# Performance work log

Hardware: AMD Instinct MI355X
Metric: run time of the kernel (lower is better)

Reference implementation:

```python
import jax, jax.numpy as jnp
import numpy as np

K = 1024
D = 512
BETA = 0.25
ALPHA = 10.0
EPS_NORM = 1e-12  # torch F.normalize eps


def _l2_normalize(x):
    n = jnp.linalg.norm(x, axis=1, keepdims=True)
    return x / jnp.maximum(n, EPS_NORM)


def setup_inputs() -> dict:
    key = jax.random.key(0)
    k1, k2 = jax.random.split(key)
    latents = jax.random.normal(k1, (16384, D), dtype=jnp.float32)
    # nn.Embedding weight init: uniform(-1/K, 1/K)
    emb_weight = jax.random.uniform(k2, (K, D), dtype=jnp.float32,
                                    minval=-1.0 / K, maxval=1.0 / K)
    return {"latents": latents, "emb_weight": emb_weight}


def reference(latents, emb_weight):
    # latents: [B, D], emb_weight: [K, D]
    ln = _l2_normalize(latents)                               # [B, D]
    # torch uses embedding.weight.data -> detached for the attention path
    cb = _l2_normalize(jax.lax.stop_gradient(emb_weight))     # [K, D]
    attention = ln @ cb.T                                     # [B, K]
    soft_assign = jax.nn.softmax(ALPHA * attention, axis=1)   # [B, K]
    quantized = soft_assign @ emb_weight                      # [B, D]

    commitment_loss = jnp.mean((jax.lax.stop_gradient(quantized) - ln) ** 2)
    embedding_loss = jnp.mean((quantized - jax.lax.stop_gradient(ln)) ** 2)
    vq_loss = commitment_loss * BETA + embedding_loss

    avg_probs = jnp.mean(soft_assign, axis=0)                 # [K]
    entropy_vq = -jnp.sum(avg_probs * jnp.log(avg_probs + 1e-10))

    argm = jnp.argmax(attention, axis=1, keepdims=True)       # [B, 1] int
    one_hot = jax.nn.one_hot(argm[:, 0], K, dtype=latents.dtype)  # [B, K]
    hard_quantized = one_hot @ emb_weight                     # [B, D]
    # attention[one_hot.bool()].mean() == mean of row-max (argmax entries)
    cluster_metric = jnp.mean(jnp.max(attention, axis=1))

    return (quantized, vq_loss, entropy_vq, argm, hard_quantized,
            soft_assign, cluster_metric)
```

## Files before the change

### kernel.cpp

```cpp
#include <hip/hip_runtime.h>
#include <math.h>

#define D     512
#define KCB   1024
#define NT    256
#define NT2   512
#define ALPHA 10.0f
#define TAU   0.008f

typedef __attribute__((ext_vector_type(8))) short short8v;
typedef __attribute__((ext_vector_type(4))) float f32x4;
typedef unsigned short us;

__device__ __forceinline__ float wave_reduce_sum(float v) {
    #pragma unroll
    for (int off = 32; off >= 1; off >>= 1) v += __shfl_xor(v, off, 64);
    return v;
}

__device__ __forceinline__ short bf16r(float x) {
    union { float f; unsigned u; } c; c.f = x;
    unsigned r = (c.u + 0x7FFFu + ((c.u >> 16) & 1u)) >> 16;
    return (short)r;
}

__global__ void k_init(float* __restrict__ avg, float* __restrict__ sse, float* __restrict__ clu) {
    int t = threadIdx.x + blockIdx.x * blockDim.x;
    if (t < KCB) avg[t] = 0.0f;
    if (t == 0) { *sse = 0.0f; *clu = 0.0f; }
}

__global__ __launch_bounds__(NT) void k_prep(const float* __restrict__ emb,
                                             us* __restrict__ cb, float* __restrict__ cbinv) {
    const int k = blockIdx.x, t = threadIdx.x;
    const int wv = t >> 6, lane = t & 63;
    float2 v = ((const float2*)(emb + (size_t)k * D))[t];
    float ss = wave_reduce_sum(v.x * v.x + v.y * v.y);
    __shared__ float part[4];
    __shared__ float s_i;
    if (lane == 0) part[wv] = ss;
    __syncthreads();
    if (t == 0) s_i = 1.0f / fmaxf(sqrtf(part[0] + part[1] + part[2] + part[3]), 1e-12f);
    __syncthreads();
    float inv = s_i;
    unsigned lo = (unsigned short)bf16r(v.x * inv);
    unsigned hi = (unsigned short)bf16r(v.y * inv);
    const int d = 2 * t;
    size_t idx = (((size_t)(k >> 4) * 16 + (d >> 5)) * 64 + ((d >> 3) & 3) * 16 + (k & 15)) * 8 + (d & 7);
    ((unsigned*)cb)[idx >> 1] = lo | (hi << 16);
    if (t == 0) cbinv[k] = inv;
}

__global__ __launch_bounds__(NT) void k_tr(const float* __restrict__ emb, us* __restrict__ embT) {
    __shared__ us tile[64][65];
    const int t = threadIdx.x;
    const int k0 = (blockIdx.x & 15) * 64;
    const int d0 = (blockIdx.x >> 4) * 64;
    {
        const int r = t >> 2, cq = t & 3;
        const float4* ep = (const float4*)(emb + (size_t)(k0 + r) * D + d0 + cq * 16);
        float4 v0 = ep[0], v1 = ep[1], v2 = ep[2], v3 = ep[3];
        us* tp = &tile[r][cq * 16];
        tp[0] = (us)bf16r(v0.x); tp[1] = (us)bf16r(v0.y); tp[2] = (us)bf16r(v0.z); tp[3] = (us)bf16r(v0.w);
        tp[4] = (us)bf16r(v1.x); tp[5] = (us)bf16r(v1.y); tp[6] = (us)bf16r(v1.z); tp[7] = (us)bf16r(v1.w);
        tp[8] = (us)bf16r(v2.x); tp[9] = (us)bf16r(v2.y); tp[10] = (us)bf16r(v2.z); tp[11] = (us)bf16r(v2.w);
        tp[12] = (us)bf16r(v3.x); tp[13] = (us)bf16r(v3.y); tp[14] = (us)bf16r(v3.z); tp[15] = (us)bf16r(v3.w);
    }
    __syncthreads();
    {
        const int rd = t >> 2, kq = t & 3;
        const int dcol = d0 + rd;
        short8v w0, w1;
        #pragma unroll
        for (int j = 0; j < 8; ++j) w0[j] = (short)tile[kq * 16 + j][rd];
        #pragma unroll
        for (int j = 0; j < 8; ++j) w1[j] = (short)tile[kq * 16 + 8 + j][rd];
        const int kb0 = k0 + kq * 16, kb1 = kb0 + 8;
        size_t i0 = (((size_t)(dcol >> 4) * 32 + (kb0 >> 5)) * 64 + ((kb0 >> 3) & 3) * 16 + (dcol & 15)) * 8;
        size_t i1 = (((size_t)(dcol >> 4) * 32 + (kb1 >> 5)) * 64 + ((kb1 >> 3) & 3) * 16 + (dcol & 15)) * 8;
        *(short8v*)(embT + i0) = w0;
        *(short8v*)(embT + i1) = w1;
    }
}

__global__ __launch_bounds__(NT2, 2) void k_attn(
    const float* __restrict__ lat, const float* __restrict__ emb,
    const us* __restrict__ cb, const float* __restrict__ cbinv,
    float* __restrict__ inv_ws, float* __restrict__ avg_ws, float* __restrict__ clu_ws,
    float* __restrict__ soft_out, float* __restrict__ argm_out, float* __restrict__ hq_out)
{
    __shared__ __align__(16) us alds[32][520];
    __shared__ float s_inv[32];
    __shared__ float s_maxp[8][32];
    __shared__ float s_amax[32];
    __shared__ float s_sump[8][32];
    __shared__ float s_den[32];
    __shared__ float s_bestv[32];
    __shared__ int   s_besti[32];
    __shared__ int   s_cnt;
    __shared__ int   s_ck[512];
    __shared__ float s_cv[512];

    const int t = threadIdx.x, wv = t >> 6, lane = t & 63;
    const int q15 = lane & 15, g = lane >> 4;
    const int b0 = blockIdx.x * 32;

    #pragma unroll
    for (int i = 0; i < 4; ++i) {
        int r = wv * 4 + i, grow = b0 + r;
        const float4* lp = (const float4*)(lat + (size_t)grow * D);
        float4 a = lp[2 * lane], b = lp[2 * lane + 1];
        float ss = a.x*a.x + a.y*a.y + a.z*a.z + a.w*a.w
                 + b.x*b.x + b.y*b.y + b.z*b.z + b.w*b.w;
        ss = wave_reduce_sum(ss);
        float inv = 1.0f / fmaxf(sqrtf(ss), 1e-12f);
        short8v w;
        w[0] = bf16r(a.x * inv); w[1] = bf16r(a.y * inv);
        w[2] = bf16r(a.z * inv); w[3] = bf16r(a.w * inv);
        w[4] = bf16r(b.x * inv); w[5] = bf16r(b.y * inv);
        w[6] = bf16r(b.z * inv); w[7] = bf16r(b.w * inv);
        *(short8v*)&alds[r][lane * 8] = w;
        if (lane == 0) { s_inv[r] = inv; inv_ws[grow] = inv; }
    }
    if (t == 0) s_cnt = 0;
    __syncthreads();

    f32x4 acc[2][8];
    #pragma unroll
    for (int m = 0; m < 2; ++m)
        #pragma unroll
        for (int ct = 0; ct < 8; ++ct) { f32x4 z = {0.f, 0.f, 0.f, 0.f}; acc[m][ct] = z; }

    const us* pBw = cb + (size_t)(wv * 8) * 16 * 512 + (size_t)lane * 8;
    for (int ks = 0; ks < 16; ++ks) {
        short8v af0 = *(const short8v*)&alds[q15][ks * 32 + g * 8];
        short8v af1 = *(const short8v*)&alds[16 + q15][ks * 32 + g * 8];
        short8v bfr[8];
        #pragma unroll
        for (int ct = 0; ct < 8; ++ct)
            bfr[ct] = *(const short8v*)(pBw + (size_t)(ct * 16 + ks) * 512);
        #pragma unroll
        for (int ct = 0; ct < 8; ++ct) {
            acc[0][ct] = __builtin_amdgcn_mfma_f32_16x16x32_bf16(af0, bfr[ct], acc[0][ct], 0, 0, 0);
            acc[1][ct] = __builtin_amdgcn_mfma_f32_16x16x32_bf16(af1, bfr[ct], acc[1][ct], 0, 0, 0);
        }
    }

    #pragma unroll
    for (int m = 0; m < 2; ++m)
        #pragma unroll
        for (int i = 0; i < 4; ++i) {
            float v = acc[m][0][i];
            #pragma unroll
            for (int ct = 1; ct < 8; ++ct) v = fmaxf(v, acc[m][ct][i]);
            #pragma unroll
            for (int off = 8; off >= 1; off >>= 1) v = fmaxf(v, __shfl_xor(v, off, 64));
            if (q15 == 0) s_maxp[wv][m * 16 + g * 4 + i] = v;
        }
    __syncthreads();
    if (t < 32) {
        float v = s_maxp[0][t];
        #pragma unroll
        for (int w = 1; w < 8; ++w) v = fmaxf(v, s_maxp[w][t]);
        s_amax[t] = v;
    }
    __syncthreads();

    #pragma unroll
    for (int m = 0; m < 2; ++m)
        #pragma unroll
        for (int i = 0; i < 4; ++i) {
            const int row = m * 16 + g * 4 + i;
            const float thr = s_amax[row] - TAU;
            #pragma unroll
            for (int ct = 0; ct < 8; ++ct) {
                if (acc[m][ct][i] >= thr) {
                    int idx = atomicAdd(&s_cnt, 1);
                    if (idx < 512) s_ck[idx] = (row << 16) | (wv * 128 + ct * 16 + q15);
                }
            }
        }
    __syncthreads();
    const int cnt = (s_cnt < 512) ? s_cnt : 512;

    for (int e = wv; e < cnt; e += 8) {
        const int pk = s_ck[e];
        const int row = pk >> 16, kk = pk & 0xFFFF;
        const float4* lp = (const float4*)(lat + (size_t)(b0 + row) * D);
        const float4* ep = (const float4*)(emb + (size_t)kk * D);
        float4 x0 = lp[2 * lane], x1 = lp[2 * lane + 1];
        float4 y0 = ep[2 * lane], y1 = ep[2 * lane + 1];
        float dp = x0.x*y0.x + x0.y*y0.y + x0.z*y0.z + x0.w*y0.w
                 + x1.x*y1.x + x1.y*y1.y + x1.z*y1.z + x1.w*y1.w;
        dp = wave_reduce_sum(dp);
        if (lane == 0) s_cv[e] = dp * s_inv[row] * cbinv[kk];
    }
    __syncthreads();
    if (t < 32) {
        float bv = -1e30f; int bi = 0x7FFFFFFF;
        for (int e = 0; e < cnt; ++e) {
            if ((s_ck[e] >> 16) == t) {
                float v = s_cv[e]; int kk = s_ck[e] & 0xFFFF;
                if (v > bv || (v == bv && kk < bi)) { bv = v; bi = kk; }
            }
        }
        s_bestv[t] = bv; s_besti[t] = bi;
        argm_out[b0 + t] = (float)bi;
    }
    __syncthreads();

    #pragma unroll
    for (int m = 0; m < 2; ++m)
        #pragma unroll
        for (int i = 0; i < 4; ++i) {
            const float bvv = s_bestv[m * 16 + g * 4 + i];
            float s = 0.f;
            #pragma unroll
            for (int ct = 0; ct < 8; ++ct) {
                float e = __expf(ALPHA * (acc[m][ct][i] - bvv));
                acc[m][ct][i] = e;
                s += e;
            }
            #pragma unroll
            for (int off = 8; off >= 1; off >>= 1) s += __shfl_xor(s, off, 64);
            if (q15 == 0) s_sump[wv][m * 16 + g * 4 + i] = s;
        }
    __syncthreads();
    if (t < 32) {
        float s = s_sump[0][t];
        #pragma unroll
        for (int w = 1; w < 8; ++w) s += s_sump[w][t];
        s_den[t] = 1.0f / s;
    }
    __syncthreads();

    float csum[8];
    #pragma unroll
    for (int ct = 0; ct < 8; ++ct) csum[ct] = 0.f;
    #pragma unroll
    for (int m = 0; m < 2; ++m)
        #pragma unroll
        for (int i = 0; i < 4; ++i) {
            const int row = m * 16 + g * 4 + i;
            const float dn = s_den[row];
            float* orow = soft_out + (size_t)(b0 + row) * KCB + wv * 128 + q15;
            #pragma unroll
            for (int ct = 0; ct < 8; ++ct) {
                float sv = acc[m][ct][i] * dn;
                orow[ct * 16] = sv;
                csum[ct] += sv;
            }
        }
    #pragma unroll
    for (int ct = 0; ct < 8; ++ct) {
        float v = csum[ct];
        v += __shfl_xor(v, 16, 64);
        v += __shfl_xor(v, 32, 64);
        csum[ct] = v;
    }
    if (lane < 16) {
        #pragma unroll
        for (int ct = 0; ct < 8; ++ct)
            atomicAdd(avg_ws + wv * 128 + ct * 16 + lane, csum[ct]);
    }
    if (t == 0) {
        float cs = 0.f;
        #pragma unroll
        for (int r = 0; r < 32; ++r) cs += s_bestv[r];
        atomicAdd(clu_ws, cs);
    }

    const float4* emb4 = (const float4*)emb;
    for (int idx = t; idx < 32 * 128; idx += NT2) {
        int r = idx >> 7, c = idx & 127;
        ((float4*)(hq_out + (size_t)(b0 + r) * D))[c] = emb4[(size_t)s_besti[r] * 128 + c];
    }
}

__global__ __launch_bounds__(NT2, 2) void k_quant(
    const float* __restrict__ lat, const us* __restrict__ embT,
    const float* __restrict__ soft_in, const float* __restrict__ inv_ws,
    float* __restrict__ q_out, float* __restrict__ sse_ws)
{
    __shared__ __align__(16) us salds[32][516];
    __shared__ float part[8];
    const int t = threadIdx.x, wv = t >> 6, lane = t & 63;
    const int q15 = lane & 15, g = lane >> 4;
    const int b0 = blockIdx.x * 32;

    f32x4 acc[2][4];
    #pragma unroll
    for (int m = 0; m < 2; ++m)
        #pragma unroll
        for (int ct = 0; ct < 4; ++ct) { f32x4 z = {0.f, 0.f, 0.f, 0.f}; acc[m][ct] = z; }

    const float4* s4 = (const float4*)soft_in;
    for (int p = 0; p < 2; ++p) {
        for (int idx = t; idx < 32 * 128; idx += NT2) {
            int r = idx >> 7, c4 = idx & 127;
            float4 v = s4[(size_t)(b0 + r) * (KCB / 4) + p * 128 + c4];
            uint2 u;
            u.x = (unsigned)(us)bf16r(v.x) | ((unsigned)(us)bf16r(v.y) << 16);
            u.y = (unsigned)(us)bf16r(v.z) | ((unsigned)(us)bf16r(v.w) << 16);
            *(uint2*)&salds[r][c4 * 4] = u;
        }
        __syncthreads();

        const us* pBw = embT + ((size_t)(wv * 128) + p * 16) * 512 + (size_t)lane * 8;
        for (int ks = 0; ks < 16; ++ks) {
            short8v af0 = *(const short8v*)&salds[q15][ks * 32 + g * 8];
            short8v af1 = *(const short8v*)&salds[16 + q15][ks * 32 + g * 8];
            short8v bfr[4];
            #pragma unroll
            for (int ct = 0; ct < 4; ++ct)
                bfr[ct] = *(const short8v*)(pBw + (size_t)(ct * 32 + ks) * 512);
            #pragma unroll
            for (int ct = 0; ct < 4; ++ct) {
                acc[0][ct] = __builtin_amdgcn_mfma_f32_16x16x32_bf16(af0, bfr[ct], acc[0][ct], 0, 0, 0);
                acc[1][ct] = __builtin_amdgcn_mfma_f32_16x16x32_bf16(af1, bfr[ct], acc[1][ct], 0, 0, 0);
            }
        }
        __syncthreads();
    }

    float sse = 0.f;
    #pragma unroll
    for (int m = 0; m < 2; ++m)
        #pragma unroll
        for (int i = 0; i < 4; ++i) {
            const int row = b0 + m * 16 + g * 4 + i;
            const float rv = inv_ws[row];
            const float* lrow = lat + (size_t)row * D + wv * 64 + q15;
            float* qrow = q_out + (size_t)row * D + wv * 64 + q15;
            #pragma unroll
            for (int ct = 0; ct < 4; ++ct) {
                float qv = acc[m][ct][i];
                qrow[ct * 16] = qv;
                float df = qv - lrow[ct * 16] * rv;
                sse += df * df;
            }
        }
    sse = wave_reduce_sum(sse);
    if (lane == 0) part[wv] = sse;
    __syncthreads();
    if (t == 0) {
        float s = 0.f;
        #pragma unroll
        for (int w = 0; w < 8; ++w) s += part[w];
        atomicAdd(sse_ws, s);
    }
}

__global__ __launch_bounds__(NT) void k_final(
    const float* __restrict__ avg_ws, const float* __restrict__ sse_ws, const float* __restrict__ clu_ws,
    float* __restrict__ out_vq, float* __restrict__ out_ent, float* __restrict__ out_cm,
    float invB, float invBD)
{
    const int t = threadIdx.x;
    float ent = 0.f;
    for (int idx = t; idx < KCB; idx += NT) {
        float pv = avg_ws[idx] * invB;
        ent -= pv * logf(pv + 1e-10f);
    }
    ent = wave_reduce_sum(ent);
    __shared__ float part[4];
    const int wv = t >> 6, lane = t & 63;
    if (lane == 0) part[wv] = ent;
    __syncthreads();
    if (t == 0) {
        *out_ent = part[0] + part[1] + part[2] + part[3];
        *out_vq  = 1.25f * (*sse_ws) * invBD;
        *out_cm  = (*clu_ws) * invB;
    }
}

extern "C" void kernel_launch(void* const* d_in, const int* in_sizes, int n_in,
                              void* d_out, int out_size, void* d_ws, size_t ws_size,
                              hipStream_t stream)
{
    const float* lat = (const float*)d_in[0];
    const float* emb = (const float*)d_in[1];
    const int B = in_sizes[0] / D;
    float* out = (float*)d_out;

    const size_t vq_off   = (size_t)B * D;
    const size_t ent_off  = vq_off + 1;
    const size_t argm_off = vq_off + 2;
    const size_t hq_off   = argm_off + (size_t)B;
    const size_t soft_off = hq_off + (size_t)B * D;
    const size_t cm_off   = soft_off + (size_t)B * KCB;

    us* cb_bf   = (us*)d_ws;
    us* embT_bf = cb_bf + (size_t)KCB * D;
    float* fbase  = (float*)(embT_bf + (size_t)D * KCB);
    float* inv_ws = fbase;
    float* cbinv  = inv_ws + B;
    float* avg_ws = cbinv + KCB;
    float* sse_ws = avg_ws + KCB;
    float* clu_ws = sse_ws + 1;

    k_init<<<4, NT, 0, stream>>>(avg_ws, sse_ws, clu_ws);
    k_prep<<<KCB, NT, 0, stream>>>(emb, cb_bf, cbinv);
    k_tr<<<(D / 64) * (KCB / 64), NT, 0, stream>>>(emb, embT_bf);
    k_attn<<<B / 32, NT2, 0, stream>>>(lat, emb, cb_bf, cbinv, inv_ws, avg_ws, clu_ws,
                                       out + soft_off, out + argm_off, out + hq_off);
    k_quant<<<B / 32, NT2, 0, stream>>>(lat, embT_bf, out + soft_off, inv_ws, out, sse_ws);
    k_final<<<1, NT, 0, stream>>>(avg_ws, sse_ws, clu_ws,
                                  out + vq_off, out + ent_off, out + cm_off,
                                  1.0f / (float)B, 1.0f / ((float)B * (float)D));
}
```

Before: 299.1 us.

## Fuse attention and quantize kernels, keeping soft-assign tile in LDS as bf16

Merges k_attn and k_quant into one kernel. The softmax probabilities are written as bf16 into a dynamic LDS pool and consumed directly by the second GEMM, so the 64MB soft_assign tensor no longer has to be re-read from global memory and the inv_ws round trip is gone. It also double-buffers the B-fragment global loads in both GEMM loops so loads overlap the MFMAs. In exchange the fused kernel carries more LDS (about 66KB of dynamic LDS) and more registers, which may lower occupancy, and the two GEMMs now run serially within each block.

```diff
diff --git a/kernel.cpp b/kernel.cpp
--- a/kernel.cpp
+++ b/kernel.cpp
@@ -7,6 +7,7 @@
 #define NT2   512
 #define ALPHA 10.0f
 #define TAU   0.008f
+#define PSTR  1040
 
 typedef __attribute__((ext_vector_type(8))) short short8v;
 typedef __attribute__((ext_vector_type(4))) float f32x4;
@@ -83,13 +84,14 @@
     }
 }
 
-__global__ __launch_bounds__(NT2, 2) void k_attn(
+__global__ __launch_bounds__(NT2, 2) void k_fused(
     const float* __restrict__ lat, const float* __restrict__ emb,
-    const us* __restrict__ cb, const float* __restrict__ cbinv,
-    float* __restrict__ inv_ws, float* __restrict__ avg_ws, float* __restrict__ clu_ws,
-    float* __restrict__ soft_out, float* __restrict__ argm_out, float* __restrict__ hq_out)
+    const us* __restrict__ cb, const us* __restrict__ embT, const float* __restrict__ cbinv,
+    float* __restrict__ avg_ws, float* __restrict__ clu_ws, float* __restrict__ sse_ws,
+    float* __restrict__ q_out, float* __restrict__ soft_out,
+    float* __restrict__ argm_out, float* __restrict__ hq_out)
 {
-    __shared__ __align__(16) us alds[32][520];
+    extern __shared__ __align__(16) us pool[];
     __shared__ float s_inv[32];
     __shared__ float s_maxp[8][32];
     __shared__ float s_amax[32];
@@ -100,16 +102,22 @@
     __shared__ int   s_cnt;
     __shared__ int   s_ck[512];
     __shared__ float s_cv[512];
+    __shared__ float part[8];
 
     const int t = threadIdx.x, wv = t >> 6, lane = t & 63;
     const int q15 = lane & 15, g = lane >> 4;
     const int b0 = blockIdx.x * 32;
 
+    float4 ra[4], rb[4];
     #pragma unroll
     for (int i = 0; i < 4; ++i) {
-        int r = wv * 4 + i, grow = b0 + r;
-        const float4* lp = (const float4*)(lat + (size_t)grow * D);
-        float4 a = lp[2 * lane], b = lp[2 * lane + 1];
+        const float4* lp = (const float4*)(lat + (size_t)(b0 + wv * 4 + i) * D);
+        ra[i] = lp[2 * lane]; rb[i] = lp[2 * lane + 1];
+    }
+    #pragma unroll
+    for (int i = 0; i < 4; ++i) {
+        int r = wv * 4 + i;
+        float4 a = ra[i], b = rb[i];
         float ss = a.x*a.x + a.y*a.y + a.z*a.z + a.w*a.w
                  + b.x*b.x + b.y*b.y + b.z*b.z + b.w*b.w;
         ss = wave_reduce_sum(ss);
@@ -119,8 +127,8 @@
         w[2] = bf16r(a.z * inv); w[3] = bf16r(a.w * inv);
         w[4] = bf16r(b.x * inv); w[5] = bf16r(b.y * inv);
         w[6] = bf16r(b.z * inv); w[7] = bf16r(b.w * inv);
-        *(short8v*)&alds[r][lane * 8] = w;
-        if (lane == 0) { s_inv[r] = inv; inv_ws[grow] = inv; }
+        *(short8v*)&pool[(size_t)r * PSTR + lane * 8] = w;
+        if (lane == 0) s_inv[r] = inv;
     }
     if (t == 0) s_cnt = 0;
     __syncthreads();
@@ -132,17 +140,29 @@
         for (int ct = 0; ct < 8; ++ct) { f32x4 z = {0.f, 0.f, 0.f, 0.f}; acc[m][ct] = z; }
 
     const us* pBw = cb + (size_t)(wv * 8) * 16 * 512 + (size_t)lane * 8;
-    for (int ks = 0; ks < 16; ++ks) {
-        short8v af0 = *(const short8v*)&alds[q15][ks * 32 + g * 8];
-        short8v af1 = *(const short8v*)&alds[16 + q15][ks * 32 + g * 8];
-        short8v bfr[8];
-        #pragma unroll
-        for (int ct = 0; ct < 8; ++ct)
-            bfr[ct] = *(const short8v*)(pBw + (size_t)(ct * 16 + ks) * 512);
+    #define LDB_A(ks, ct) (*(const short8v*)(pBw + (size_t)((ct) * 16 + (ks)) * 512))
+    #define LDA_A(row, ks) (*(const short8v*)&pool[(size_t)(row) * PSTR + (ks) * 32 + g * 8])
+
+    short8v bE[8], bO[8];
+    #pragma unroll
+    for (int ct = 0; ct < 8; ++ct) bE[ct] = LDB_A(0, ct);
+    for (int ks = 0; ks < 16; ks += 2) {
+        #pragma unroll
+        for (int ct = 0; ct < 8; ++ct) bO[ct] = LDB_A(ks + 1, ct);
+        short8v af0 = LDA_A(q15, ks), af1 = LDA_A(16 + q15, ks);
         #pragma unroll
         for (int ct = 0; ct < 8; ++ct) {
-            acc[0][ct] = __builtin_amdgcn_mfma_f32_16x16x32_bf16(af0, bfr[ct], acc[0][ct], 0, 0, 0);
-            acc[1][ct] = __builtin_amdgcn_mfma_f32_16x16x32_bf16(af1, bfr[ct], acc[1][ct], 0, 0, 0);
+            acc[0][ct] = __builtin_amdgcn_mfma_f32_16x16x32_bf16(af0, bE[ct], acc[0][ct], 0, 0, 0);
+            acc[1][ct] = __builtin_amdgcn_mfma_f32_16x16x32_bf16(af1, bE[ct], acc[1][ct], 0, 0, 0);
+        }
+        const int ksn = (ks + 2 < 16) ? ks + 2 : 0;
+        #pragma unroll
+        for (int ct = 0; ct < 8; ++ct) bE[ct] = LDB_A(ksn, ct);
+        af0 = LDA_A(q15, ks + 1); af1 = LDA_A(16 + q15, ks + 1);
+        #pragma unroll
+        for (int ct = 0; ct < 8; ++ct) {
+            acc[0][ct] = __builtin_amdgcn_mfma_f32_16x16x32_bf16(af0, bO[ct], acc[0][ct], 0, 0, 0);
+            acc[1][ct] = __builtin_amdgcn_mfma_f32_16x16x32_bf16(af1, bO[ct], acc[1][ct], 0, 0, 0);
         }
     }
 
@@ -244,10 +264,12 @@
             const int row = m * 16 + g * 4 + i;
             const float dn = s_den[row];
             float* orow = soft_out + (size_t)(b0 + row) * KCB + wv * 128 + q15;
+            us* prow = &pool[(size_t)row * PSTR + wv * 128 + q15];
             #pragma unroll
             for (int ct = 0; ct < 8; ++ct) {
                 float sv = acc[m][ct][i] * dn;
                 orow[ct * 16] = sv;
+                prow[ct * 16] = (us)bf16r(sv);
                 csum[ct] += sv;
             }
         }
@@ -269,58 +291,47 @@
         for (int r = 0; r < 32; ++r) cs += s_bestv[r];
         atomicAdd(clu_ws, cs);
     }
+    __syncthreads();
 
     const float4* emb4 = (const float4*)emb;
-    for (int idx = t; idx < 32 * 128; idx += NT2) {
+    #pragma unroll
+    for (int u = 0; u < 8; ++u) {
+        int idx = t + u * NT2;
         int r = idx >> 7, c = idx & 127;
         ((float4*)(hq_out + (size_t)(b0 + r) * D))[c] = emb4[(size_t)s_besti[r] * 128 + c];
     }
-}
-
-__global__ __launch_bounds__(NT2, 2) void k_quant(
-    const float* __restrict__ lat, const us* __restrict__ embT,
-    const float* __restrict__ soft_in, const float* __restrict__ inv_ws,
-    float* __restrict__ q_out, float* __restrict__ sse_ws)
-{
-    __shared__ __align__(16) us salds[32][516];
-    __shared__ float part[8];
-    const int t = threadIdx.x, wv = t >> 6, lane = t & 63;
-    const int q15 = lane & 15, g = lane >> 4;
-    const int b0 = blockIdx.x * 32;
-
-    f32x4 acc[2][4];
-    #pragma unroll
-    for (int m = 0; m < 2; ++m)
-        #pragma unroll
-        for (int ct = 0; ct < 4; ++ct) { f32x4 z = {0.f, 0.f, 0.f, 0.f}; acc[m][ct] = z; }
-
-    const float4* s4 = (const float4*)soft_in;
-    for (int p = 0; p < 2; ++p) {
-        for (int idx = t; idx < 32 * 128; idx += NT2) {
-            int r = idx >> 7, c4 = idx & 127;
-            float4 v = s4[(size_t)(b0 + r) * (KCB / 4) + p * 128 + c4];
-            uint2 u;
-            u.x = (unsigned)(us)bf16r(v.x) | ((unsigned)(us)bf16r(v.y) << 16);
-            u.y = (unsigned)(us)bf16r(v.z) | ((unsigned)(us)bf16r(v.w) << 16);
-            *(uint2*)&salds[r][c4 * 4] = u;
-        }
-        __syncthreads();
-
-        const us* pBw = embT + ((size_t)(wv * 128) + p * 16) * 512 + (size_t)lane * 8;
-        for (int ks = 0; ks < 16; ++ks) {
-            short8v af0 = *(const short8v*)&salds[q15][ks * 32 + g * 8];
-            short8v af1 = *(const short8v*)&salds[16 + q15][ks * 32 + g * 8];
-            short8v bfr[4];
-            #pragma unroll
-            for (int ct = 0; ct < 4; ++ct)
-                bfr[ct] = *(const short8v*)(pBw + (size_t)(ct * 32 + ks) * 512);
-            #pragma unroll
-            for (int ct = 0; ct < 4; ++ct) {
-                acc[0][ct] = __builtin_amdgcn_mfma_f32_16x16x32_bf16(af0, bfr[ct], acc[0][ct], 0, 0, 0);
-                acc[1][ct] = __builtin_amdgcn_mfma_f32_16x16x32_bf16(af1, bfr[ct], acc[1][ct], 0, 0, 0);
-            }
-        }
-        __syncthreads();
+
+    f32x4 qac[2][4];
+    #pragma unroll
+    for (int m = 0; m < 2; ++m)
+        #pragma unroll
+        for (int ct = 0; ct < 4; ++ct) { f32x4 z = {0.f, 0.f, 0.f, 0.f}; qac[m][ct] = z; }
+
+    const us* pBq = embT + (size_t)(wv * 128) * 512 + (size_t)lane * 8;
+    #define LDB_Q(ks, ct) (*(const short8v*)(pBq + (size_t)((ct) * 32 + (ks)) * 512))
+    #define LDA_Q(row, ks) (*(const short8v*)&pool[(size_t)(row) * PSTR + (ks) * 32 + g * 8])
+
+    short8v qE[4], qO[4];
+    #pragma unroll
+    for (int ct = 0; ct < 4; ++ct) qE[ct] = LDB_Q(0, ct);
+    for (int ks = 0; ks < 32; ks += 2) {
+        #pragma unroll
+        for (int ct = 0; ct < 4; ++ct) qO[ct] = LDB_Q(ks + 1, ct);
+        short8v af0 = LDA_Q(q15, ks), af1 = LDA_Q(16 + q15, ks);
+        #pragma unroll
+        for (int ct = 0; ct < 4; ++ct) {
+            qac[0][ct] = __builtin_amdgcn_mfma_f32_16x16x32_bf16(af0, qE[ct], qac[0][ct], 0, 0, 0);
+            qac[1][ct] = __builtin_amdgcn_mfma_f32_16x16x32_bf16(af1, qE[ct], qac[1][ct], 0, 0, 0);
+        }
+        const int ksn = (ks + 2 < 32) ? ks + 2 : 0;
+        #pragma unroll
+        for (int ct = 0; ct < 4; ++ct) qE[ct] = LDB_Q(ksn, ct);
+        af0 = LDA_Q(q15, ks + 1); af1 = LDA_Q(16 + q15, ks + 1);
+        #pragma unroll
+        for (int ct = 0; ct < 4; ++ct) {
+            qac[0][ct] = __builtin_amdgcn_mfma_f32_16x16x32_bf16(af0, qO[ct], qac[0][ct], 0, 0, 0);
+            qac[1][ct] = __builtin_amdgcn_mfma_f32_16x16x32_bf16(af1, qO[ct], qac[1][ct], 0, 0, 0);
+        }
     }
 
     float sse = 0.f;
@@ -328,13 +339,14 @@
     for (int m = 0; m < 2; ++m)
         #pragma unroll
         for (int i = 0; i < 4; ++i) {
-            const int row = b0 + m * 16 + g * 4 + i;
-            const float rv = inv_ws[row];
+            const int rloc = m * 16 + g * 4 + i;
+            const int row = b0 + rloc;
+            const float rv = s_inv[rloc];
             const float* lrow = lat + (size_t)row * D + wv * 64 + q15;
             float* qrow = q_out + (size_t)row * D + wv * 64 + q15;
             #pragma unroll
             for (int ct = 0; ct < 4; ++ct) {
-                float qv = acc[m][ct][i];
+                float qv = qac[m][ct][i];
                 qrow[ct * 16] = qv;
                 float df = qv - lrow[ct * 16] * rv;
                 sse += df * df;
@@ -349,6 +361,10 @@
         for (int w = 0; w < 8; ++w) s += part[w];
         atomicAdd(sse_ws, s);
     }
+    #undef LDB_A
+    #undef LDA_A
+    #undef LDB_Q
+    #undef LDA_Q
 }
 
 __global__ __launch_bounds__(NT) void k_final(
@@ -393,18 +409,19 @@
     us* cb_bf   = (us*)d_ws;
     us* embT_bf = cb_bf + (size_t)KCB * D;
     float* fbase  = (float*)(embT_bf + (size_t)D * KCB);
-    float* inv_ws = fbase;
-    float* cbinv  = inv_ws + B;
+    float* cbinv  = fbase;
     float* avg_ws = cbinv + KCB;
     float* sse_ws = avg_ws + KCB;
     float* clu_ws = sse_ws + 1;
 
+    const int lds_bytes = 32 * PSTR * 2;
+
     k_init<<<4, NT, 0, stream>>>(avg_ws, sse_ws, clu_ws);
     k_prep<<<KCB, NT, 0, stream>>>(emb, cb_bf, cbinv);
     k_tr<<<(D / 64) * (KCB / 64), NT, 0, stream>>>(emb, embT_bf);
-    k_attn<<<B / 32, NT2, 0, stream>>>(lat, emb, cb_bf, cbinv, inv_ws, avg_ws, clu_ws,
-                                       out + soft_off, out + argm_off, out + hq_off);
-    k_quant<<<B / 32, NT2, 0, stream>>>(lat, embT_bf, out + soft_off, inv_ws, out, sse_ws);
+    k_fused<<<B / 32, NT2, lds_bytes, stream>>>(lat, emb, cb_bf, embT_bf, cbinv,
+                                                avg_ws, clu_ws, sse_ws,
+                                                out, out + soft_off, out + argm_off, out + hq_off);
     k_final<<<1, NT, 0, stream>>>(avg_ws, sse_ws, clu_ws,
                                   out + vq_off, out + ent_off, out + cm_off,
                                   1.0f / (float)B, 1.0f / ((float)B * (float)D));
```

Result: no change. 294.3 us (-1.6%).
